# Optimization experiments

Measured on AMD Instinct MI355X. Metric: run time of the kernel, lower is better.

The kernel has to match this reference:

```python
import jax, jax.numpy as jnp
import numpy as np

S = 64    # shapelets_size
N = 256   # num_shapelets
C = 3     # in_channels
B = 64
L = 2048


def setup_inputs() -> dict:
    key = jax.random.key(0)
    kx, ks = jax.random.split(key)
    x = jax.random.normal(kx, (B, C, L), dtype=jnp.float32)
    shapelets = jax.random.normal(ks, (C, N, S), dtype=jnp.float32)
    return {"x": x, "shapelets": shapelets}


def reference(x, shapelets):
    # x: (B, C, L); shapelets: (C, N, S)
    W = x.shape[2] - S + 1  # number of sliding windows
    # unfold: (B, C, W, S)
    idx = jnp.arange(W)[:, None] + jnp.arange(S)[None, :]
    win = x[:, :, idx]
    # cdist with mm-based euclidean: d^2 = |a|^2 + |b|^2 - 2 a.b
    win_sq = jnp.sum(win * win, axis=-1)                 # (B, C, W)
    shp_sq = jnp.sum(shapelets * shapelets, axis=-1)     # (C, N)
    cross = jnp.einsum('bcws,cns->bcwn', win, shapelets)  # (B, C, W, N)
    d2 = win_sq[..., None] + shp_sq[None, :, None, :] - 2.0 * cross
    d = jnp.sqrt(jnp.maximum(d2, 0.0))                   # (B, C, W, N)
    # sum over channels, keepdim -> (B, 1, W, N); transpose -> (B, 1, N, W); min over W
    summed = jnp.sum(d, axis=1, keepdims=True)
    out = jnp.min(jnp.swapaxes(summed, 2, 3), axis=3)    # (B, 1, N)
    return out
```

## Files before the change

kernel.cpp:

```cpp
#include <hip/hip_runtime.h>
#include <hip/hip_fp16.h>


typedef float  v4f __attribute__((ext_vector_type(4)));
typedef short  v8s __attribute__((ext_vector_type(8)));
typedef unsigned short u16;
typedef unsigned int   u32;
typedef unsigned long long u64;

#define S_ 64
#define N_ 256
#define C_ 3
#define L_ 2048
#define W_ 1985
#define WL 1024
#define NCH 274
#define THREADS 256
#define OUT_ELEMS 16384

__device__ __forceinline__ u16 f2bf(float f) {
    u32 u = __builtin_bit_cast(u32, f);
    return (u16)((u + 0x7FFFu + ((u >> 16) & 1u)) >> 16);
}
__device__ __forceinline__ float bf2f(u16 b) {
    return __builtin_bit_cast(float, ((u32)b) << 16);
}

__global__ __launch_bounds__(256)
void init_out_kernel(u32* __restrict__ out_u) {
    int i = blockIdx.x * 256 + threadIdx.x;
    if (i < OUT_ELEMS) out_u[i] = 0x7F800000u;
}

__global__ __launch_bounds__(THREADS, 4)
void shapelet_min_kernel(const float* __restrict__ x,
                         const float* __restrict__ shp,
                         u32* __restrict__ out_u)
{
    __shared__ u64 xcopy[C_][4][NCH];
    __shared__ __half hwq[C_][WL];

    const int tid  = threadIdx.x;
    const int wave = tid >> 6;
    const int lane = tid & 63;
    const int m    = lane & 15;
    const int q    = lane >> 4;
    const int wh   = blockIdx.x & 1;
    const int nb   = (blockIdx.x >> 1) & 7;
    const int b    = blockIdx.x >> 4;
    const int n0   = nb << 5;
    const int wstart = wh * WL;

    u16* scratch = (u16*)&xcopy[0][0][0];
    #pragma unroll
    for (int k = 0; k < 6; ++k) {
        int idx = tid + k * THREADS;
        int sq = idx & 15;
        int n  = (idx >> 4) & 31;
        int c  = idx >> 9;
        v4f v = *(const v4f*)(shp + ((size_t)(c * N_ + n0 + n) * S_ + (sq << 2)));
        u64 pk = (u64)f2bf(v[0]) | ((u64)f2bf(v[1]) << 16)
               | ((u64)f2bf(v[2]) << 32) | ((u64)f2bf(v[3]) << 48);
        *(u64*)(scratch + ((c * 32 + n) * 72 + (sq << 2))) = pk;
    }
    __syncthreads();

    v8s   bfr[C_][2][2];
    float hs[C_][2];
    #pragma unroll
    for (int c = 0; c < C_; ++c) {
        #pragma unroll
        for (int nt = 0; nt < 2; ++nt) {
            float sacc = 0.f;
            #pragma unroll
            for (int h = 0; h < 2; ++h) {
                v8s f = *(const v8s*)(scratch + ((c * 32 + nt * 16 + m) * 72 + h * 32 + q * 8));
                bfr[c][nt][h] = f;
                #pragma unroll
                for (int j = 0; j < 8; ++j) {
                    float e = bf2f((u16)f[j]);
                    sacc += e * e;
                }
            }
            sacc += __shfl_xor(sacc, 16);
            sacc += __shfl_xor(sacc, 32);
            hs[c][nt] = -0.5f * sacc;
        }
    }
    __syncthreads();

    {
        const float* xb = x + (size_t)b * (C_ * L_);
        #pragma unroll
        for (int k = 0; k < 4; ++k) {
            int gi = tid + k * THREADS;
            if (gi < C_ * NCH) {
                int c = gi / NCH;
                int t = gi - c * NCH;
                int e = t << 2;
                int ge = wstart + e;
                float f[4];
                if (ge + 3 < L_) {
                    v4f v = *(const v4f*)(xb + c * L_ + ge);
                    f[0] = v[0]; f[1] = v[1]; f[2] = v[2]; f[3] = v[3];
                } else {
                    #pragma unroll
                    for (int i = 0; i < 4; ++i)
                        f[i] = (ge + i < L_) ? xb[c * L_ + ge + i] : 0.f;
                }
                u16 u[4];
                #pragma unroll
                for (int i = 0; i < 4; ++i) u[i] = f2bf(f[i]);
                #pragma unroll
                for (int r = 0; r < 4; ++r) {
                    u16* cp = (u16*)&xcopy[c][r][0];
                    #pragma unroll
                    for (int i = 0; i < 4; ++i) {
                        int pos = e + i - r;
                        if (pos >= 0) cp[pos] = u[i];
                    }
                }
            }
        }
    }
    __syncthreads();

    #pragma unroll
    for (int c = 0; c < C_; ++c) {
        const u64* cp0 = &xcopy[c][0][0];
        float e[68];
        #pragma unroll
        for (int kk = 0; kk < 17; ++kk) {
            u64 ch = cp0[tid + kk];
            e[kk * 4 + 0] = bf2f((u16)(ch));
            e[kk * 4 + 1] = bf2f((u16)(ch >> 16));
            e[kk * 4 + 2] = bf2f((u16)(ch >> 32));
            e[kk * 4 + 3] = bf2f((u16)(ch >> 48));
        }
        float s0 = 0.f;
        #pragma unroll
        for (int i = 0; i < 64; ++i) s0 += e[i] * e[i];
        float s1 = s0 - e[0] * e[0] + e[64] * e[64];
        float s2 = s1 - e[1] * e[1] + e[65] * e[65];
        float s3 = s2 - e[2] * e[2] + e[66] * e[66];
        union { u64 u; __half h[4]; } hp;
        hp.h[0] = __float2half(-0.5f * s0); hp.h[1] = __float2half(-0.5f * s1);
        hp.h[2] = __float2half(-0.5f * s2); hp.h[3] = __float2half(-0.5f * s3);
        *(u64*)&hwq[c][tid << 2] = hp.u;
    }
    __syncthreads();

    float mins[2] = {1e30f, 1e30f};

    #pragma unroll 1
    for (int it = 0; it < 8; ++it) {
        const int wb = it * 128 + wave * 32;
        if (wstart + wb >= W_) continue;

        float sums[2][2][4];
        #pragma unroll
        for (int mt = 0; mt < 2; ++mt)
            #pragma unroll
            for (int nt = 0; nt < 2; ++nt)
                #pragma unroll
                for (int g = 0; g < 4; ++g) sums[mt][nt][g] = 0.f;

        #pragma unroll
        for (int c = 0; c < C_; ++c) {
            v4f acc[2][2];
            #pragma unroll
            for (int mt = 0; mt < 2; ++mt) {
                union { u64 u; __half h4[4]; } wq;
                wq.u = *(const u64*)&hwq[c][wb + mt * 16 + q * 4];
                #pragma unroll
                for (int g = 0; g < 4; ++g) {
                    float hv = __half2float(wq.h4[g]);
                    acc[mt][0][g] = hv + hs[c][0];
                    acc[mt][1][g] = hv + hs[c][1];
                }
            }
            #pragma unroll
            for (int h = 0; h < 2; ++h) {
                v8s afr[2];
                #pragma unroll
                for (int mt = 0; mt < 2; ++mt) {
                    int p0 = wb + mt * 16 + m + h * 32 + q * 8;
                    int r  = m & 3;
                    int T  = (p0 - r) >> 2;
                    const u64* cp = &xcopy[c][r][0];
                    union { u64 u[2]; v8s v; } tmp;
                    tmp.u[0] = cp[T];
                    tmp.u[1] = cp[T + 1];
                    afr[mt] = tmp.v;
                }
                #pragma unroll
                for (int mt = 0; mt < 2; ++mt)
                    #pragma unroll
                    for (int nt = 0; nt < 2; ++nt)
                        acc[mt][nt] = __builtin_amdgcn_mfma_f32_16x16x32_bf16(
                            afr[mt], bfr[c][nt][h], acc[mt][nt], 0, 0, 0);
            }
            #pragma unroll
            for (int mt = 0; mt < 2; ++mt)
                #pragma unroll
                for (int nt = 0; nt < 2; ++nt)
                    #pragma unroll
                    for (int g = 0; g < 4; ++g)
                        sums[mt][nt][g] += __builtin_amdgcn_sqrtf(fmaxf(-acc[mt][nt][g], 0.f));
        }
        #pragma unroll
        for (int mt = 0; mt < 2; ++mt) {
            #pragma unroll
            for (int g = 0; g < 4; ++g) {
                bool ok = (wstart + wb + mt * 16 + q * 4 + g) < W_;
                #pragma unroll
                for (int nt = 0; nt < 2; ++nt) {
                    float vv = ok ? sums[mt][nt][g] : 1e30f;
                    mins[nt] = fminf(mins[nt], vv);
                }
            }
        }
    }

    #pragma unroll
    for (int nt = 0; nt < 2; ++nt) {
        mins[nt] = fminf(mins[nt], __shfl_xor(mins[nt], 16));
        mins[nt] = fminf(mins[nt], __shfl_xor(mins[nt], 32));
    }
    if (lane < 16) {
        #pragma unroll
        for (int nt = 0; nt < 2; ++nt) {
            float v = mins[nt] * 1.41421356237f;
            atomicMin(out_u + ((size_t)b * N_ + n0 + nt * 16 + m), __float_as_uint(v));
        }
    }
}

extern "C" void kernel_launch(void* const* d_in, const int* in_sizes, int n_in,
                              void* d_out, int out_size, void* d_ws, size_t ws_size,
                              hipStream_t stream) {
    const float* x   = (const float*)d_in[0];
    const float* shp = (const float*)d_in[1];
    u32* out_u       = (u32*)d_out;

    hipLaunchKernelGGL(init_out_kernel, dim3((OUT_ELEMS + 255) / 256), dim3(256), 0, stream, out_u);
    hipLaunchKernelGGL(shapelet_min_kernel, dim3(1024), dim3(THREADS), 0, stream,
                       x, (const float*)shp, out_u);
}
```

Measured before the change: 92.26 us.

## Precompute bf16 shifted x copies and norms in a prep kernel, split windows finer

Adds a prep kernel that converts x to bf16 once and writes 8 shifted copies per row, computes the window norms as fp16 and converts the shapelets to bf16 with their norms into workspace. It also initialises the output. The main kernel then only copies the precomputed data into LDS, reads 16-byte aligned A fragments directly, and runs on 2048 blocks with 512-window halves. Each block reduces its minima across waves in LDS so only one atomicMin is issued per shapelet per block. This removes redundant per-block conversion and norm work, but adds workspace traffic and an extra kernel dependency.

After: 104.0 us. 12.8% more time.

```diff
diff --git a/kernel.cpp b/kernel.cpp
--- a/kernel.cpp
+++ b/kernel.cpp
@@ -3,20 +3,24 @@
 
 
 typedef float  v4f __attribute__((ext_vector_type(4)));
+typedef unsigned int v4u __attribute__((ext_vector_type(4)));
 typedef short  v8s __attribute__((ext_vector_type(8)));
 typedef unsigned short u16;
 typedef unsigned int   u32;
 typedef unsigned long long u64;
 
-#define S_ 64
 #define N_ 256
 #define C_ 3
 #define L_ 2048
 #define W_ 1985
-#define WL 1024
-#define NCH 274
-#define THREADS 256
-#define OUT_ELEMS 16384
+#define XPAD 2176
+#define CPY_U64 150
+#define WL 512
+
+#define OFF_GX   0u
+#define OFF_HW   6684672u
+#define OFF_SHP  7471104u
+#define OFF_HS   7569408u
 
 __device__ __forceinline__ u16 f2bf(float f) {
     u32 u = __builtin_bit_cast(u32, f);
@@ -25,135 +29,160 @@
 __device__ __forceinline__ float bf2f(u16 b) {
     return __builtin_bit_cast(float, ((u32)b) << 16);
 }
+__device__ __forceinline__ u64 pack4(v4f v) {
+    return (u64)f2bf(v[0]) | ((u64)f2bf(v[1]) << 16)
+         | ((u64)f2bf(v[2]) << 32) | ((u64)f2bf(v[3]) << 48);
+}
 
 __global__ __launch_bounds__(256)
-void init_out_kernel(u32* __restrict__ out_u) {
-    int i = blockIdx.x * 256 + threadIdx.x;
-    if (i < OUT_ELEMS) out_u[i] = 0x7F800000u;
-}
-
-__global__ __launch_bounds__(THREADS, 4)
-void shapelet_min_kernel(const float* __restrict__ x,
-                         const float* __restrict__ shp,
+void prep_kernel(const float* __restrict__ x, const float* __restrict__ shp,
+                 u16* __restrict__ gx, u16* __restrict__ ghw,
+                 u16* __restrict__ gshp, float* __restrict__ ghs,
+                 u32* __restrict__ out_u)
+{
+    const int blk = blockIdx.x, tid = threadIdx.x;
+    if (blk < 192) {
+        __shared__ u16 xb[2240];
+        const int b = blk / 3, c = blk % 3;
+        const float* xr = x + (size_t)(b * 3 + c) * L_;
+        {
+            v4f a0 = *(const v4f*)(xr + tid * 8);
+            v4f a1 = *(const v4f*)(xr + tid * 8 + 4);
+            ((u64*)xb)[tid * 2]     = pack4(a0);
+            ((u64*)xb)[tid * 2 + 1] = pack4(a1);
+            if (tid < 24) ((u64*)xb)[512 + tid] = 0;
+        }
+        __syncthreads();
+        {
+            const int r = tid >> 5, u0 = tid & 31;
+            const bool odd = (r & 1);
+            const int wadd = r >> 1;
+            u16* grow = gx + ((size_t)(b * 3 + c) * 8 + r) * XPAD;
+            const u32* lw = (const u32*)xb;
+            #pragma unroll 1
+            for (int i = 0; i < 9; ++i) {
+                int u = u0 + i * 32;
+                if (u < 272) {
+                    u32 w[5];
+                    #pragma unroll
+                    for (int j = 0; j < 5; ++j) w[j] = lw[u * 4 + wadd + j];
+                    v4u o;
+                    #pragma unroll
+                    for (int j = 0; j < 4; ++j) {
+                        u32 sh = (w[j] >> 16) | (w[j + 1] << 16);
+                        o[j] = odd ? sh : w[j];
+                    }
+                    *(v4u*)(grow + u * 8) = o;
+                }
+            }
+        }
+        {
+            float e[80];
+            #pragma unroll
+            for (int j = 0; j < 20; ++j) {
+                u64 ch = ((const u64*)xb)[tid * 2 + j];
+                e[j * 4 + 0] = bf2f((u16)(ch));
+                e[j * 4 + 1] = bf2f((u16)(ch >> 16));
+                e[j * 4 + 2] = bf2f((u16)(ch >> 32));
+                e[j * 4 + 3] = bf2f((u16)(ch >> 48));
+            }
+            float s = 0.f;
+            #pragma unroll
+            for (int i = 0; i < 64; ++i) s += e[i] * e[i];
+            union { v4u v; __half h[8]; } hp;
+            hp.h[0] = __float2half(-0.5f * s);
+            #pragma unroll
+            for (int k = 1; k < 8; ++k) {
+                s += e[63 + k] * e[63 + k] - e[k - 1] * e[k - 1];
+                hp.h[k] = __float2half(-0.5f * s);
+            }
+            *(v4u*)(ghw + (size_t)(b * 3 + c) * L_ + tid * 8) = hp.v;
+        }
+    } else if (blk < 195) {
+        const int c = blk - 192;
+        const int n = tid;
+        const float* row = shp + ((size_t)c * N_ + n) * 64;
+        float sacc = 0.f;
+        #pragma unroll
+        for (int k = 0; k < 8; ++k) {
+            v4f a0 = *(const v4f*)(row + k * 8);
+            v4f a1 = *(const v4f*)(row + k * 8 + 4);
+            u64 p0 = pack4(a0), p1 = pack4(a1);
+            union { u64 u[2]; v4u v; } st; st.u[0] = p0; st.u[1] = p1;
+            *(v4u*)(gshp + ((size_t)c * N_ + n) * 64 + k * 8) = st.v;
+            #pragma unroll
+            for (int j = 0; j < 4; ++j) {
+                float e0 = bf2f((u16)(p0 >> (16 * j)));
+                float e1 = bf2f((u16)(p1 >> (16 * j)));
+                sacc += e0 * e0 + e1 * e1;
+            }
+        }
+        ghs[c * N_ + n] = -0.5f * sacc;
+    } else {
+        int i = (blk - 195) * 256 + tid;
+        out_u[i] = 0x7F800000u;
+    }
+}
+
+__global__ __launch_bounds__(256, 4)
+void shapelet_min_kernel(const u16* __restrict__ gx, const u16* __restrict__ ghw,
+                         const u16* __restrict__ gshp, const float* __restrict__ ghs,
                          u32* __restrict__ out_u)
 {
-    __shared__ u64 xcopy[C_][4][NCH];
-    __shared__ __half hwq[C_][WL];
+    __shared__ __align__(16) u64 xcopy[C_ * 8 * CPY_U64];
+    __shared__ __align__(16) __half hwq[C_ * WL];
+    __shared__ float red[4][32];
 
     const int tid  = threadIdx.x;
     const int wave = tid >> 6;
     const int lane = tid & 63;
     const int m    = lane & 15;
     const int q    = lane >> 4;
-    const int wh   = blockIdx.x & 1;
-    const int nb   = (blockIdx.x >> 1) & 7;
-    const int b    = blockIdx.x >> 4;
+    const int r    = m & 7;
+    const int a    = m >> 3;
+    const int wh   = blockIdx.x & 3;
+    const int nb   = (blockIdx.x >> 2) & 7;
+    const int b    = blockIdx.x >> 5;
     const int n0   = nb << 5;
     const int wstart = wh * WL;
 
-    u16* scratch = (u16*)&xcopy[0][0][0];
-    #pragma unroll
-    for (int k = 0; k < 6; ++k) {
-        int idx = tid + k * THREADS;
-        int sq = idx & 15;
-        int n  = (idx >> 4) & 31;
-        int c  = idx >> 9;
-        v4f v = *(const v4f*)(shp + ((size_t)(c * N_ + n0 + n) * S_ + (sq << 2)));
-        u64 pk = (u64)f2bf(v[0]) | ((u64)f2bf(v[1]) << 16)
-               | ((u64)f2bf(v[2]) << 32) | ((u64)f2bf(v[3]) << 48);
-        *(u64*)(scratch + ((c * 32 + n) * 72 + (sq << 2))) = pk;
-    }
-    __syncthreads();
-
-    v8s   bfr[C_][2][2];
+    {
+        const u16* gxb = gx + (size_t)b * 24 * XPAD;
+        #pragma unroll
+        for (int i = 0; i < 8; ++i) {
+            int idx = tid + (i << 8);
+            if (idx < 1800) {
+                int cr = idx / 75;
+                int u  = idx - cr * 75;
+                v4u v = *(const v4u*)(gxb + cr * XPAD + wstart + u * 8);
+                *(v4u*)((char*)xcopy + cr * 1200 + u * 16) = v;
+            }
+        }
+    }
+    if (tid < 192) {
+        int c = tid >> 6, u = tid & 63;
+        v4u v = *(const v4u*)(ghw + (size_t)(b * 3 + c) * L_ + wstart + u * 8);
+        *(v4u*)((char*)hwq + c * 1024 + u * 16) = v;
+    }
+    v8s bfr[C_][2][2];
     float hs[C_][2];
     #pragma unroll
-    for (int c = 0; c < C_; ++c) {
+    for (int c = 0; c < C_; ++c)
         #pragma unroll
         for (int nt = 0; nt < 2; ++nt) {
-            float sacc = 0.f;
-            #pragma unroll
-            for (int h = 0; h < 2; ++h) {
-                v8s f = *(const v8s*)(scratch + ((c * 32 + nt * 16 + m) * 72 + h * 32 + q * 8));
-                bfr[c][nt][h] = f;
-                #pragma unroll
-                for (int j = 0; j < 8; ++j) {
-                    float e = bf2f((u16)f[j]);
-                    sacc += e * e;
-                }
-            }
-            sacc += __shfl_xor(sacc, 16);
-            sacc += __shfl_xor(sacc, 32);
-            hs[c][nt] = -0.5f * sacc;
-        }
-    }
+            int n = n0 + nt * 16 + m;
+            hs[c][nt] = ghs[c * N_ + n];
+            #pragma unroll
+            for (int h = 0; h < 2; ++h)
+                bfr[c][nt][h] = *(const v8s*)(gshp + ((size_t)(c * N_ + n) * 64 + h * 32 + q * 8));
+        }
     __syncthreads();
 
-    {
-        const float* xb = x + (size_t)b * (C_ * L_);
-        #pragma unroll
-        for (int k = 0; k < 4; ++k) {
-            int gi = tid + k * THREADS;
-            if (gi < C_ * NCH) {
-                int c = gi / NCH;
-                int t = gi - c * NCH;
-                int e = t << 2;
-                int ge = wstart + e;
-                float f[4];
-                if (ge + 3 < L_) {
-                    v4f v = *(const v4f*)(xb + c * L_ + ge);
-                    f[0] = v[0]; f[1] = v[1]; f[2] = v[2]; f[3] = v[3];
-                } else {
-                    #pragma unroll
-                    for (int i = 0; i < 4; ++i)
-                        f[i] = (ge + i < L_) ? xb[c * L_ + ge + i] : 0.f;
-                }
-                u16 u[4];
-                #pragma unroll
-                for (int i = 0; i < 4; ++i) u[i] = f2bf(f[i]);
-                #pragma unroll
-                for (int r = 0; r < 4; ++r) {
-                    u16* cp = (u16*)&xcopy[c][r][0];
-                    #pragma unroll
-                    for (int i = 0; i < 4; ++i) {
-                        int pos = e + i - r;
-                        if (pos >= 0) cp[pos] = u[i];
-                    }
-                }
-            }
-        }
-    }
-    __syncthreads();
-
-    #pragma unroll
-    for (int c = 0; c < C_; ++c) {
-        const u64* cp0 = &xcopy[c][0][0];
-        float e[68];
-        #pragma unroll
-        for (int kk = 0; kk < 17; ++kk) {
-            u64 ch = cp0[tid + kk];
-            e[kk * 4 + 0] = bf2f((u16)(ch));
-            e[kk * 4 + 1] = bf2f((u16)(ch >> 16));
-            e[kk * 4 + 2] = bf2f((u16)(ch >> 32));
-            e[kk * 4 + 3] = bf2f((u16)(ch >> 48));
-        }
-        float s0 = 0.f;
-        #pragma unroll
-        for (int i = 0; i < 64; ++i) s0 += e[i] * e[i];
-        float s1 = s0 - e[0] * e[0] + e[64] * e[64];
-        float s2 = s1 - e[1] * e[1] + e[65] * e[65];
-        float s3 = s2 - e[2] * e[2] + e[66] * e[66];
-        union { u64 u; __half h[4]; } hp;
-        hp.h[0] = __float2half(-0.5f * s0); hp.h[1] = __float2half(-0.5f * s1);
-        hp.h[2] = __float2half(-0.5f * s2); hp.h[3] = __float2half(-0.5f * s3);
-        *(u64*)&hwq[c][tid << 2] = hp.u;
-    }
-    __syncthreads();
-
     float mins[2] = {1e30f, 1e30f};
+    const int laneoff = q + a;
 
     #pragma unroll 1
-    for (int it = 0; it < 8; ++it) {
+    for (int it = 0; it < 4; ++it) {
         const int wb = it * 128 + wave * 32;
         if (wstart + wb >= W_) continue;
 
@@ -171,7 +200,7 @@
             #pragma unroll
             for (int mt = 0; mt < 2; ++mt) {
                 union { u64 u; __half h4[4]; } wq;
-                wq.u = *(const u64*)&hwq[c][wb + mt * 16 + q * 4];
+                wq.u = *(const u64*)&hwq[c * WL + wb + mt * 16 + q * 4];
                 #pragma unroll
                 for (int g = 0; g < 4; ++g) {
                     float hv = __half2float(wq.h4[g]);
@@ -179,19 +208,14 @@
                     acc[mt][1][g] = hv + hs[c][1];
                 }
             }
+            const char* cb = (const char*)xcopy + (c * 8 + r) * 1200;
             #pragma unroll
             for (int h = 0; h < 2; ++h) {
                 v8s afr[2];
                 #pragma unroll
                 for (int mt = 0; mt < 2; ++mt) {
-                    int p0 = wb + mt * 16 + m + h * 32 + q * 8;
-                    int r  = m & 3;
-                    int T  = (p0 - r) >> 2;
-                    const u64* cp = &xcopy[c][r][0];
-                    union { u64 u[2]; v8s v; } tmp;
-                    tmp.u[0] = cp[T];
-                    tmp.u[1] = cp[T + 1];
-                    afr[mt] = tmp.v;
+                    int k = (wb >> 3) + mt * 2 + h * 4 + laneoff;
+                    afr[mt] = *(const v8s*)(cb + k * 16);
                 }
                 #pragma unroll
                 for (int mt = 0; mt < 2; ++mt)
@@ -227,12 +251,13 @@
         mins[nt] = fminf(mins[nt], __shfl_xor(mins[nt], 16));
         mins[nt] = fminf(mins[nt], __shfl_xor(mins[nt], 32));
     }
-    if (lane < 16) {
-        #pragma unroll
-        for (int nt = 0; nt < 2; ++nt) {
-            float v = mins[nt] * 1.41421356237f;
-            atomicMin(out_u + ((size_t)b * N_ + n0 + nt * 16 + m), __float_as_uint(v));
-        }
+    if (lane < 16) { red[wave][m] = mins[0]; red[wave][16 + m] = mins[1]; }
+    __syncthreads();
+    if (tid < 32) {
+        float v = fminf(fminf(red[0][tid], red[1][tid]),
+                        fminf(red[2][tid], red[3][tid]));
+        atomicMin(out_u + (size_t)b * N_ + n0 + tid,
+                  __float_as_uint(v * 1.41421356237f));
     }
 }
 
@@ -243,7 +268,14 @@
     const float* shp = (const float*)d_in[1];
     u32* out_u       = (u32*)d_out;
 
-    hipLaunchKernelGGL(init_out_kernel, dim3((OUT_ELEMS + 255) / 256), dim3(256), 0, stream, out_u);
-    hipLaunchKernelGGL(shapelet_min_kernel, dim3(1024), dim3(THREADS), 0, stream,
-                       x, (const float*)shp, out_u);
-}
+    char* ws = (char*)d_ws;
+    u16*   gx   = (u16*)(ws + OFF_GX);
+    u16*   ghw  = (u16*)(ws + OFF_HW);
+    u16*   gshp = (u16*)(ws + OFF_SHP);
+    float* ghs  = (float*)(ws + OFF_HS);
+
+    hipLaunchKernelGGL(prep_kernel, dim3(259), dim3(256), 0, stream,
+                       x, shp, gx, ghw, gshp, ghs, out_u);
+    hipLaunchKernelGGL(shapelet_min_kernel, dim3(2048), dim3(256), 0, stream,
+                       gx, ghw, gshp, ghs, out_u);
+}
```
